# Kernel optimization log

Hardware: AMD Instinct MI355X
Metric: run time of the kernel (lower is better)

The kernel has to match this reference:

```python
import jax, jax.numpy as jnp
import numpy as np

B, L, D_MODEL = 2, 2048, 1024
D_STATE, D_CONV, EXPAND = 8, 4, 2
D_INNER = EXPAND * D_MODEL          # 2048
DT_RANK = (D_MODEL + 15) // 16      # 64


def setup_inputs() -> dict:
    key = jax.random.key(0)
    ks = jax.random.split(key, 8)
    s = 0.02
    x = jax.random.normal(ks[0], (B, L, D_MODEL), dtype=jnp.float32)
    W_in = jax.random.normal(ks[1], (D_MODEL, 2 * D_INNER), dtype=jnp.float32) * s
    dw_kernel = jax.random.normal(ks[2], (D_CONV, D_INNER), dtype=jnp.float32) * s  # depthwise
    pw_kernel = jax.random.normal(ks[3], (D_INNER, D_INNER), dtype=jnp.float32) * s  # pointwise
    conv_bias = jnp.zeros((D_INNER,), dtype=jnp.float32)
    W_x = jax.random.normal(ks[4], (D_INNER, DT_RANK + 2 * D_STATE), dtype=jnp.float32) * s
    W_dt = jax.random.normal(ks[5], (DT_RANK, D_INNER), dtype=jnp.float32) * s
    b_dt = jnp.zeros((D_INNER,), dtype=jnp.float32)
    # A = repeat(range(1..d_state), d_inner).reshape(d_inner, d_state), stored as log
    A_init = np.repeat(np.arange(1, D_STATE + 1, dtype=np.float32), D_INNER).reshape(D_INNER, D_STATE)
    A_log = jnp.asarray(np.log(A_init))
    D = jnp.ones((D_INNER,), dtype=jnp.float32)
    W_out = jax.random.normal(ks[6], (D_INNER, D_MODEL), dtype=jnp.float32) * s
    return {"x": x, "W_in": W_in, "dw_kernel": dw_kernel, "pw_kernel": pw_kernel,
            "conv_bias": conv_bias, "W_x": W_x, "W_dt": W_dt, "b_dt": b_dt,
            "A_log": A_log, "D": D, "W_out": W_out}


def reference(x, W_in, dw_kernel, pw_kernel, conv_bias, W_x, W_dt, b_dt, A_log, D, W_out):
    d_inner, d_state = A_log.shape
    dt_rank = W_dt.shape[0]
    d_conv = dw_kernel.shape[0]
    bsz = x.shape[0]

    xz = x @ W_in                                   # [B,L,2*di]
    x_in, z = jnp.split(xz, 2, axis=-1)             # each [B,L,di]

    # causal separable conv: depthwise (causal pad) -> pointwise -> swish
    xp = jnp.pad(x_in, ((0, 0), (d_conv - 1, 0), (0, 0)))
    xc = jax.lax.conv_general_dilated(
        xp, dw_kernel[:, None, :], window_strides=(1,), padding='VALID',
        dimension_numbers=('NWC', 'WIO', 'NWC'), feature_group_count=d_inner)
    xc = jax.nn.silu(xc @ pw_kernel + conv_bias)    # [B,L,di]

    x_dbl = xc @ W_x                                # [B,L,dt_rank+2*ds]
    delta = x_dbl[..., :dt_rank]
    Bm = x_dbl[..., dt_rank:dt_rank + d_state]      # [B,L,ds]
    C = x_dbl[..., dt_rank + d_state:]              # [B,L,ds]
    delta = jax.nn.softplus(delta @ W_dt + b_dt)    # [B,L,di]

    A = -jnp.exp(A_log)                             # [di,ds]
    deltaA = jnp.exp(jnp.einsum('bld,dn->bldn', delta, A))       # [B,L,di,ds]
    deltaB_u = jnp.einsum('bld,bln,bld->bldn', delta, Bm, xc)    # [B,L,di,ds]

    def step(h, inp):
        dA_t, dBu_t, C_t = inp
        h = dA_t * h + dBu_t                        # [B,di,ds]
        y_t = jnp.einsum('bn,bdn->bd', C_t, h)      # [B,di]
        return h, y_t

    h0 = jnp.zeros((bsz, d_inner, d_state), dtype=x.dtype)
    elems = (deltaA.transpose(1, 0, 2, 3), deltaB_u.transpose(1, 0, 2, 3), C.transpose(1, 0, 2))
    _, ys = jax.lax.scan(step, h0, elems)           # ys: [L,B,di]
    y = ys.transpose(1, 0, 2)                       # [B,L,di]

    y = y + xc * D
    y = y * jax.nn.silu(z)
    return y @ W_out                                # [B,L,d_model]
```

## Files before the change

kernel.cpp:

```cpp
#include <hip/hip_runtime.h>
#include <math.h>

#define Bb 2
#define Ll 2048
#define DMODEL 1024
#define DINNER 2048
#define DSTATE 8
#define DTRANK 64
#define DCONV 4
#define MM (Bb*Ll)
#define NCH 64
#define CL 32
#define G3_KCH 8
#define G3_KC (DINNER / G3_KCH)

typedef __attribute__((ext_vector_type(8))) short    bf16x8;
typedef __attribute__((ext_vector_type(4))) float    f32x4;

__device__ __forceinline__ float silu_f(float x) {
    return x / (1.0f + __expf(-x));
}
__device__ __forceinline__ float softplus_f(float x) {
    return fmaxf(x, 0.0f) + log1pf(__expf(-fabsf(x)));
}
__device__ __forceinline__ unsigned short f2bf(float f) {
    unsigned int u = __float_as_uint(f);
    u += 0x7fffu + ((u >> 16) & 1u);
    return (unsigned short)(u >> 16);
}
__device__ __forceinline__ float bf2f(unsigned short u) {
    return __uint_as_float(((unsigned int)u) << 16);
}
__device__ __forceinline__ void async_cp16(const unsigned short* g, unsigned short* l) {
    __builtin_amdgcn_global_load_lds(
        (const __attribute__((address_space(1))) void*)g,
        (__attribute__((address_space(3))) void*)l, 16, 0, 0);
}

template <int EPI, int NW, int TN, typename OT, int RX = 0, int RY = 1>
__global__ __launch_bounds__(NW * 64, 4) void mfma_gemm(
    const unsigned short* __restrict__ A, const unsigned short* __restrict__ Bt,
    OT* __restrict__ C, OT* __restrict__ C2, int nsplit,
    int M, int N, int K, int lda, int ldb, int ldc,
    const float* __restrict__ bias)
{
    constexpr int NT   = NW * 64;
    constexpr int WNC  = NW / 2;
    constexpr int WNE  = TN / WNC;
    constexpr int NJ   = WNE / 16;
    constexpr int RPP  = NT / 4;
    constexpr int APASS = 128 / RPP;
    constexpr int BPASS = TN / RPP;

    __shared__ unsigned short As[2][128 * 32];
    __shared__ unsigned short Bs[2][TN * 32];

    int bxx = blockIdx.x, byy = blockIdx.y;
    if constexpr (RX > 0) {
        const int f = blockIdx.y * gridDim.x + blockIdx.x;
        const int c = f & 7, q = f >> 3;
        const int rgw = gridDim.x / RX;
        bxx = (c % rgw) * RX + (q % RX);
        byy = (c / rgw) * RY + (q / RX);
    }
    const int bm = byy * 128;
    const int bn = bxx * TN;
    const int tid  = threadIdx.x;
    const int w    = tid >> 6;
    const int lane = tid & 63;
    const int wm = (w / WNC) * 64;
    const int wn = (w % WNC) * WNE;
    const int lr = lane & 15;
    const int lq = lane >> 4;

    const int row  = tid >> 2;
    const int sp   = tid & 3;
    const int slog = sp ^ ((row >> 1) & 3);
    const unsigned short* gA = A  + (size_t)(bm + row) * lda + slog * 8;
    const unsigned short* gB = Bt + (size_t)(bn + row) * ldb + slog * 8;
    const int st = tid * 8;

    const int fsw = (lq ^ ((lr >> 1) & 3)) * 8;

    f32x4 acc[4][NJ];
#pragma unroll
    for (int i = 0; i < 4; ++i)
#pragma unroll
        for (int j = 0; j < NJ; ++j) acc[i][j] = (f32x4){0.f, 0.f, 0.f, 0.f};

#pragma unroll
    for (int p = 0; p < APASS; ++p)
        async_cp16(gA + (size_t)p * RPP * lda, &As[0][p * RPP * 32 + st]);
#pragma unroll
    for (int p = 0; p < BPASS; ++p)
        async_cp16(gB + (size_t)p * RPP * ldb, &Bs[0][p * RPP * 32 + st]);

    int cur = 0;
    for (int k0 = 0; k0 < K; k0 += 32, cur ^= 1) {
        __syncthreads();
        const int nk = k0 + 32;
        if (nk < K) {
            const int nb = cur ^ 1;
#pragma unroll
            for (int p = 0; p < APASS; ++p)
                async_cp16(gA + (size_t)p * RPP * lda + nk, &As[nb][p * RPP * 32 + st]);
#pragma unroll
            for (int p = 0; p < BPASS; ++p)
                async_cp16(gB + (size_t)p * RPP * ldb + nk, &Bs[nb][p * RPP * 32 + st]);
        }

        bf16x8 a[4], b[NJ];
#pragma unroll
        for (int i = 0; i < 4; ++i)
            a[i] = *(const bf16x8*)&As[cur][(wm + i * 16 + lr) * 32 + fsw];
#pragma unroll
        for (int j = 0; j < NJ; ++j)
            b[j] = *(const bf16x8*)&Bs[cur][(wn + j * 16 + lr) * 32 + fsw];
#pragma unroll
        for (int i = 0; i < 4; ++i)
#pragma unroll
            for (int j = 0; j < NJ; ++j)
                acc[i][j] = __builtin_amdgcn_mfma_f32_16x16x32_bf16(
                    a[i], b[j], acc[i][j], 0, 0, 0);
    }

#pragma unroll
    for (int i = 0; i < 4; ++i) {
        const int row0 = bm + wm + i * 16 + lq * 4;
#pragma unroll
        for (int j = 0; j < NJ; ++j) {
            const int col = bn + wn + j * 16 + lr;
            OT* Cb; int colb;
            if (col < nsplit) { Cb = C; colb = col; }
            else              { Cb = C2; colb = col - nsplit; }
            float bv = (EPI != 0) ? bias[col] : 0.0f;
#pragma unroll
            for (int r = 0; r < 4; ++r) {
                float v = acc[i][j][r];
                if (EPI == 1) v = silu_f(v + bv);
                if (EPI == 2) v = softplus_f(v + bv);
                if (sizeof(OT) == 2)
                    Cb[(size_t)(row0 + r) * ldc + colb] = (OT)f2bf(v);
                else
                    Cb[(size_t)(row0 + r) * ldc + colb] = (OT)v;
            }
        }
    }
}

template <bool I1, bool I2, int VMA, int VMB>
__device__ __forceinline__ void g1_tile(
    int kt, const unsigned short* __restrict__ gA,
    const unsigned short* __restrict__ gB, int lda, int ldb,
    unsigned short* As, unsigned short* Bs, int st,
    int wm, int wn, int lr, int fsw, f32x4 (&acc)[8][4])
{
    const int cur = kt & 1;
    const int sb0 = (cur << 1) * 8192;
    const int sb1 = ((cur << 1) | 1) * 8192;
    const int nb1 = ((kt + 1) & 1) << 1;
    const int nb2 = ((kt + 2) & 1) << 1;
    bf16x8 a[4], b[4];

#pragma unroll
    for (int i = 0; i < 4; ++i)
        a[i] = *(const bf16x8*)&As[sb0 + (wm + i * 16 + lr) * 32 + fsw];
#pragma unroll
    for (int j = 0; j < 4; ++j)
        b[j] = *(const bf16x8*)&Bs[sb0 + (wn + j * 16 + lr) * 32 + fsw];
    if (I1) {
        const unsigned short* s = gA + (kt + 1) * 64 + 32;
        unsigned short* d = &As[(nb1 | 1) * 8192 + st];
        async_cp16(s, d);
        async_cp16(s + (size_t)128 * lda, d + 4096);
        __builtin_amdgcn_sched_barrier(0);
    }
    __builtin_amdgcn_s_barrier();
    asm volatile("s_waitcnt lgkmcnt(0)" ::: "memory");
    __builtin_amdgcn_sched_barrier(0);
    __builtin_amdgcn_s_setprio(1);
#pragma unroll
    for (int i = 0; i < 4; ++i)
#pragma unroll
        for (int j = 0; j < 4; ++j)
            acc[i][j] = __builtin_amdgcn_mfma_f32_16x16x32_bf16(
                a[i], b[j], acc[i][j], 0, 0, 0);
    __builtin_amdgcn_s_setprio(0);
    __builtin_amdgcn_s_barrier();

#pragma unroll
    for (int i = 0; i < 4; ++i)
        a[i] = *(const bf16x8*)&As[sb0 + (wm + (4 + i) * 16 + lr) * 32 + fsw];
    if (I1) {
        const unsigned short* s = gB + (kt + 1) * 64 + 32;
        unsigned short* d = &Bs[(nb1 | 1) * 8192 + st];
        async_cp16(s, d);
        async_cp16(s + (size_t)128 * ldb, d + 4096);
        __builtin_amdgcn_sched_barrier(0);
    }
    __builtin_amdgcn_s_barrier();
    asm volatile("s_waitcnt lgkmcnt(0)" ::: "memory");
    __builtin_amdgcn_sched_barrier(0);
    __builtin_amdgcn_s_setprio(1);
#pragma unroll
    for (int i = 0; i < 4; ++i)
#pragma unroll
        for (int j = 0; j < 4; ++j)
            acc[4 + i][j] = __builtin_amdgcn_mfma_f32_16x16x32_bf16(
                a[i], b[j], acc[4 + i][j], 0, 0, 0);
    __builtin_amdgcn_s_setprio(0);
    asm volatile("s_waitcnt vmcnt(%0)" :: "n"(VMA) : "memory");
    __builtin_amdgcn_s_barrier();

#pragma unroll
    for (int i = 0; i < 4; ++i)
        a[i] = *(const bf16x8*)&As[sb1 + (wm + i * 16 + lr) * 32 + fsw];
#pragma unroll
    for (int j = 0; j < 4; ++j)
        b[j] = *(const bf16x8*)&Bs[sb1 + (wn + j * 16 + lr) * 32 + fsw];
    if (I2) {
        const unsigned short* s = gA + (kt + 2) * 64;
        unsigned short* d = &As[nb2 * 8192 + st];
        async_cp16(s, d);
        async_cp16(s + (size_t)128 * lda, d + 4096);
        __builtin_amdgcn_sched_barrier(0);
    }
    __builtin_amdgcn_s_barrier();
    asm volatile("s_waitcnt lgkmcnt(0)" ::: "memory");
    __builtin_amdgcn_sched_barrier(0);
    __builtin_amdgcn_s_setprio(1);
#pragma unroll
    for (int i = 0; i < 4; ++i)
#pragma unroll
        for (int j = 0; j < 4; ++j)
            acc[i][j] = __builtin_amdgcn_mfma_f32_16x16x32_bf16(
                a[i], b[j], acc[i][j], 0, 0, 0);
    __builtin_amdgcn_s_setprio(0);
    __builtin_amdgcn_s_barrier();

#pragma unroll
    for (int i = 0; i < 4; ++i)
        a[i] = *(const bf16x8*)&As[sb1 + (wm + (4 + i) * 16 + lr) * 32 + fsw];
    if (I2) {
        const unsigned short* s = gB + (kt + 2) * 64;
        unsigned short* d = &Bs[nb2 * 8192 + st];
        async_cp16(s, d);
        async_cp16(s + (size_t)128 * ldb, d + 4096);
        __builtin_amdgcn_sched_barrier(0);
    }
    __builtin_amdgcn_s_barrier();
    asm volatile("s_waitcnt lgkmcnt(0)" ::: "memory");
    __builtin_amdgcn_sched_barrier(0);
    __builtin_amdgcn_s_setprio(1);
#pragma unroll
    for (int i = 0; i < 4; ++i)
#pragma unroll
        for (int j = 0; j < 4; ++j)
            acc[4 + i][j] = __builtin_amdgcn_mfma_f32_16x16x32_bf16(
                a[i], b[j], acc[4 + i][j], 0, 0, 0);
    __builtin_amdgcn_s_setprio(0);
    asm volatile("s_waitcnt vmcnt(%0)" :: "n"(VMB) : "memory");
    __builtin_amdgcn_s_barrier();
}

__global__ __launch_bounds__(512, 2) void gemm256_g1(
    const unsigned short* __restrict__ A, const unsigned short* __restrict__ Bt,
    unsigned short* __restrict__ Cx, unsigned short* __restrict__ Cz,
    int K, int lda, int ldb, int ldc, int nsplit)
{
    __shared__ unsigned short As[4 * 8192];
    __shared__ unsigned short Bs[4 * 8192];

    int bx, by;
    {
        const int f = blockIdx.y * gridDim.x + blockIdx.x;
        const int c = f & 7, q = f >> 3;
        const int rgw = gridDim.x >> 3;
        bx = (c % rgw) * 8 + (q & 7);
        by = (c / rgw) * 4 + (q >> 3);
    }
    const int bm = by * 256, bn = bx * 256;
    const int tid  = threadIdx.x;
    const int lane = tid & 63;
    const int w    = tid >> 6;
    const int wm = (w >> 2) << 7;
    const int wn = (w & 3) << 6;
    const int lr = lane & 15;
    const int lq = lane >> 4;
    const int fsw = (lq ^ ((lr >> 1) & 3)) * 8;

    const int row  = tid >> 2;
    const int slog = (tid & 3) ^ ((row >> 1) & 3);
    const unsigned short* gA = A  + (size_t)(bm + row) * lda + slog * 8;
    const unsigned short* gB = Bt + (size_t)(bn + row) * ldb + slog * 8;
    const int st = tid * 8;
    const int NT = K >> 6;

    f32x4 acc[8][4];
#pragma unroll
    for (int i = 0; i < 8; ++i)
#pragma unroll
        for (int j = 0; j < 4; ++j) acc[i][j] = (f32x4){0.f, 0.f, 0.f, 0.f};

    auto stg = [&](const unsigned short* g, int ld, unsigned short* d) {
        async_cp16(g, d);
        async_cp16(g + (size_t)128 * ld, d + 4096);
    };
    stg(gA,      lda, As + 0 * 8192 + st);
    __builtin_amdgcn_sched_barrier(0);
    stg(gB,      ldb, Bs + 0 * 8192 + st);
    __builtin_amdgcn_sched_barrier(0);
    stg(gA + 32, lda, As + 1 * 8192 + st);
    __builtin_amdgcn_sched_barrier(0);
    stg(gB + 32, ldb, Bs + 1 * 8192 + st);
    __builtin_amdgcn_sched_barrier(0);
    stg(gA + 64, lda, As + 2 * 8192 + st);
    __builtin_amdgcn_sched_barrier(0);
    stg(gB + 64, ldb, Bs + 2 * 8192 + st);
    asm volatile("s_waitcnt vmcnt(8)" ::: "memory");
    __builtin_amdgcn_sched_barrier(0);
    __builtin_amdgcn_s_barrier();

    for (int kt = 0; kt + 2 < NT; ++kt)
        g1_tile<true, true, 8, 8>(kt, gA, gB, lda, ldb,
                                  As, Bs, st, wm, wn, lr, fsw, acc);
    g1_tile<true,  false, 8, 4>(NT - 2, gA, gB, lda, ldb,
                                As, Bs, st, wm, wn, lr, fsw, acc);
    g1_tile<false, false, 0, 0>(NT - 1, gA, gB, lda, ldb,
                                As, Bs, st, wm, wn, lr, fsw, acc);

#pragma unroll
    for (int i = 0; i < 8; ++i) {
        const int row0 = bm + wm + i * 16 + lq * 4;
#pragma unroll
        for (int j = 0; j < 4; ++j) {
            const int col = bn + wn + j * 16 + lr;
            unsigned short* Cb; int colb;
            if (col < nsplit) { Cb = Cx; colb = col; }
            else              { Cb = Cz; colb = col - nsplit; }
#pragma unroll
            for (int r = 0; r < 4; ++r)
                Cb[(size_t)(row0 + r) * ldc + colb] = f2bf(acc[i][j][r]);
        }
    }
}

template <bool I1, bool I2, int VMA, int VMB>
__device__ __forceinline__ void g2_tile(
    int kt, const unsigned short* __restrict__ gA,
    const unsigned short* __restrict__ gB, int lda, int ldb,
    unsigned short* As, unsigned short* Bs, int st,
    int wm, int wn, int lr, int fsw, f32x4 (&acc)[4][4])
{
    const int cur = kt & 1;
    const int sa0 = (cur << 1) * 8192;
    const int sa1 = ((cur << 1) | 1) * 8192;
    const int sb0 = (cur << 1) * 4096;
    const int sb1 = ((cur << 1) | 1) * 4096;
    const int nb1 = (((kt + 1) & 1) << 1) | 1;
    const int nb2 = ((kt + 2) & 1) << 1;
    bf16x8 a[4], b[4];

#pragma unroll
    for (int i = 0; i < 4; ++i)
        a[i] = *(const bf16x8*)&As[sa0 + (wm + i * 16 + lr) * 32 + fsw];
#pragma unroll
    for (int j = 0; j < 4; ++j)
        b[j] = *(const bf16x8*)&Bs[sb0 + (wn + j * 16 + lr) * 32 + fsw];
    if (I1) {
        const unsigned short* sA = gA + (kt + 1) * 64 + 32;
        unsigned short* dA = &As[nb1 * 8192 + st];
        async_cp16(sA, dA);
        async_cp16(sA + (size_t)128 * lda, dA + 4096);
        async_cp16(gB + (kt + 1) * 64 + 32, &Bs[nb1 * 4096 + st]);
        __builtin_amdgcn_sched_barrier(0);
    }
    __builtin_amdgcn_s_barrier();
    asm volatile("s_waitcnt lgkmcnt(0)" ::: "memory");
    __builtin_amdgcn_sched_barrier(0);
    __builtin_amdgcn_s_setprio(1);
#pragma unroll
    for (int i = 0; i < 4; ++i)
#pragma unroll
        for (int j = 0; j < 4; ++j)
            acc[i][j] = __builtin_amdgcn_mfma_f32_16x16x32_bf16(
                a[i], b[j], acc[i][j], 0, 0, 0);
    __builtin_amdgcn_s_setprio(0);
    asm volatile("s_waitcnt vmcnt(%0)" :: "n"(VMA) : "memory");
    __builtin_amdgcn_s_barrier();

#pragma unroll
    for (int i = 0; i < 4; ++i)
        a[i] = *(const bf16x8*)&As[sa1 + (wm + i * 16 + lr) * 32 + fsw];
#pragma unroll
    for (int j = 0; j < 4; ++j)
        b[j] = *(const bf16x8*)&Bs[sb1 + (wn + j * 16 + lr) * 32 + fsw];
    if (I2) {
        const unsigned short* sA = gA + (kt + 2) * 64;
        unsigned short* dA = &As[nb2 * 8192 + st];
        async_cp16(sA, dA);
        async_cp16(sA + (size_t)128 * lda, dA + 4096);
        async_cp16(gB + (kt + 2) * 64, &Bs[nb2 * 4096 + st]);
        __builtin_amdgcn_sched_barrier(0);
    }
    __builtin_amdgcn_s_barrier();
    asm volatile("s_waitcnt lgkmcnt(0)" ::: "memory");
    __builtin_amdgcn_sched_barrier(0);
    __builtin_amdgcn_s_setprio(1);
#pragma unroll
    for (int i = 0; i < 4; ++i)
#pragma unroll
        for (int j = 0; j < 4; ++j)
            acc[i][j] = __builtin_amdgcn_mfma_f32_16x16x32_bf16(
                a[i], b[j], acc[i][j], 0, 0, 0);
    __builtin_amdgcn_s_setprio(0);
    asm volatile("s_waitcnt vmcnt(%0)" :: "n"(VMB) : "memory");
    __builtin_amdgcn_s_barrier();
}

template <int EPI, typename OT>
__global__ __launch_bounds__(512, 2) void gemm256x128(
    const unsigned short* __restrict__ A, const unsigned short* __restrict__ Bt,
    OT* __restrict__ C, int K, int lda, int ldb, int ldc,
    const float* __restrict__ bias)
{
    __shared__ unsigned short As[4 * 8192];
    __shared__ unsigned short Bs[4 * 4096];

    int bx, by;
    {
        const int f = blockIdx.y * gridDim.x + blockIdx.x;
        const int c = f & 7, q = f >> 3;
        const int rgw = gridDim.x >> 3;
        bx = (c % rgw) * 8 + (q & 7);
        by = (c / rgw) * 4 + (q >> 3);
    }
    const int bm = by * 256, bn = bx * 128;
    const int tid  = threadIdx.x;
    const int lane = tid & 63;
    const int w    = tid >> 6;
    const int wm = (w >> 1) << 6;
    const int wn = (w & 1) << 6;
    const int lr = lane & 15;
    const int lq = lane >> 4;
    const int fsw = (lq ^ ((lr >> 1) & 3)) * 8;

    const int row  = tid >> 2;
    const int slog = (tid & 3) ^ ((row >> 1) & 3);
    const unsigned short* gA = A  + (size_t)(bm + row) * lda + slog * 8;
    const unsigned short* gB = Bt + (size_t)(bn + row) * ldb + slog * 8;
    const int st = tid * 8;
    const int NT = K >> 6;

    f32x4 acc[4][4];
#pragma unroll
    for (int i = 0; i < 4; ++i)
#pragma unroll
        for (int j = 0; j < 4; ++j) acc[i][j] = (f32x4){0.f, 0.f, 0.f, 0.f};

    auto stg = [&](int ko, int slot) {
        const unsigned short* sA = gA + ko;
        unsigned short* dA = &As[slot * 8192 + st];
        async_cp16(sA, dA);
        async_cp16(sA + (size_t)128 * lda, dA + 4096);
        async_cp16(gB + ko, &Bs[slot * 4096 + st]);
    };
    stg(0, 0);
    __builtin_amdgcn_sched_barrier(0);
    stg(32, 1);
    __builtin_amdgcn_sched_barrier(0);
    stg(64, 2);
    asm volatile("s_waitcnt vmcnt(6)" ::: "memory");
    __builtin_amdgcn_sched_barrier(0);
    __builtin_amdgcn_s_barrier();

    for (int kt = 0; kt + 2 < NT; ++kt)
        g2_tile<true, true, 6, 6>(kt, gA, gB, lda, ldb,
                                  As, Bs, st, wm, wn, lr, fsw, acc);
    g2_tile<true,  false, 6, 3>(NT - 2, gA, gB, lda, ldb,
                                As, Bs, st, wm, wn, lr, fsw, acc);
    g2_tile<false, false, 0, 0>(NT - 1, gA, gB, lda, ldb,
                                As, Bs, st, wm, wn, lr, fsw, acc);

#pragma unroll
    for (int i = 0; i < 4; ++i) {
        const int row0 = bm + wm + i * 16 + lq * 4;
#pragma unroll
        for (int j = 0; j < 4; ++j) {
            const int col = bn + wn + j * 16 + lr;
            float bv = (EPI != 0) ? bias[col] : 0.0f;
#pragma unroll
            for (int r = 0; r < 4; ++r) {
                float v = acc[i][j][r];
                if (EPI == 1) v = silu_f(v + bv);
                if (EPI == 2) v = softplus_f(v + bv);
                if (sizeof(OT) == 2)
                    C[(size_t)(row0 + r) * ldc + col] = (OT)f2bf(v);
                else
                    C[(size_t)(row0 + r) * ldc + col] = (OT)v;
            }
        }
    }
}

__global__ __launch_bounds__(256) void prep_all(
    const float* __restrict__ x, const float* __restrict__ W_in,
    const float* __restrict__ pwk, const float* __restrict__ W_out,
    const float* __restrict__ W_dt,
    unsigned short* __restrict__ x_bf, unsigned short* __restrict__ Wint,
    unsigned short* __restrict__ pw_t, unsigned short* __restrict__ Woutt,
    unsigned short* __restrict__ Wdtt)
{
    const int b = blockIdx.x;
    const int t = threadIdx.x;
    if (b < 4096) {
        int i = b * 1024 + t * 4;
        float4 v = *(const float4*)&x[i];
        ushort4 o;
        o.x = f2bf(v.x); o.y = f2bf(v.y); o.z = f2bf(v.z); o.w = f2bf(v.w);
        *(ushort4*)&x_bf[i] = o;
        return;
    }
    const float* src; unsigned short* dst; int R, C, c0, r0;
    if (b < 8192) {
        int bi = b - 4096; src = W_in; dst = Wint; R = 1024; C = 4096;
        c0 = (bi & 127) * 32; r0 = (bi >> 7) * 32;
    } else if (b < 12288) {
        int bi = b - 8192; src = pwk; dst = pw_t; R = 2048; C = 2048;
        c0 = (bi & 63) * 32; r0 = (bi >> 6) * 32;
    } else if (b < 14336) {
        int bi = b - 12288; src = W_out; dst = Woutt; R = 2048; C = 1024;
        c0 = (bi & 31) * 32; r0 = (bi >> 5) * 32;
    } else {
        int bi = b - 14336; src = W_dt; dst = Wdtt; R = 64; C = 2048;
        c0 = (bi & 63) * 32; r0 = (bi >> 6) * 32;
    }
    __shared__ float tile[32][33];
    const int tx = t & 31;
    const int ty = t >> 5;
#pragma unroll
    for (int i = 0; i < 32; i += 8)
        tile[ty + i][tx] = src[(size_t)(r0 + ty + i) * C + c0 + tx];
    __syncthreads();
#pragma unroll
    for (int i = 0; i < 32; i += 8)
        dst[(size_t)(c0 + ty + i) * R + r0 + tx] = f2bf(tile[tx][ty + i]);
}

__global__ __launch_bounds__(256) void g3_splitk(
    const unsigned short* __restrict__ xc, const float* __restrict__ Wx,
    float* __restrict__ part)
{
    __shared__ float As[16][68];
    __shared__ float Bs[16][85];
    const int m0 = blockIdx.x * 64;
    const int kb = blockIdx.y * G3_KC;
    const int t = threadIdx.x;
    const int tr = t >> 4;
    const int tc = t & 15;

    const int arow = t >> 2;
    const int ak4  = (t & 3) * 4;
    const int bk   = t >> 4;
    const int bc   = (t & 15) * 5;

    float acc[4][5];
#pragma unroll
    for (int r = 0; r < 4; ++r)
#pragma unroll
        for (int c = 0; c < 5; ++c) acc[r][c] = 0.0f;

    for (int k0 = 0; k0 < G3_KC; k0 += 16) {
        ushort4 av = *(const ushort4*)&xc[(size_t)(m0 + arow) * DINNER + kb + k0 + ak4];
        float bv[5];
#pragma unroll
        for (int q = 0; q < 5; ++q)
            bv[q] = Wx[(size_t)(kb + k0 + bk) * 80 + bc + q];
        __syncthreads();
        As[ak4 + 0][arow] = bf2f(av.x);
        As[ak4 + 1][arow] = bf2f(av.y);
        As[ak4 + 2][arow] = bf2f(av.z);
        As[ak4 + 3][arow] = bf2f(av.w);
#pragma unroll
        for (int q = 0; q < 5; ++q) Bs[bk][bc + q] = bv[q];
        __syncthreads();
#pragma unroll
        for (int k = 0; k < 16; ++k) {
            float a[4], b[5];
#pragma unroll
            for (int r = 0; r < 4; ++r) a[r] = As[k][tr * 4 + r];
#pragma unroll
            for (int c = 0; c < 5; ++c) b[c] = Bs[k][tc * 5 + c];
#pragma unroll
            for (int r = 0; r < 4; ++r)
#pragma unroll
                for (int c = 0; c < 5; ++c)
                    acc[r][c] = fmaf(a[r], b[c], acc[r][c]);
        }
    }
#pragma unroll
    for (int r = 0; r < 4; ++r)
#pragma unroll
        for (int c = 0; c < 5; ++c)
            part[((size_t)blockIdx.y * MM + m0 + tr * 4 + r) * 80 + tc * 5 + c] = acc[r][c];
}

__global__ __launch_bounds__(256) void g3_reduce(
    const float* __restrict__ part, float* __restrict__ xdbl,
    unsigned short* __restrict__ xdbl64)
{
    int i = (blockIdx.x * 256 + threadIdx.x) * 4;
    if (i >= MM * 80) return;
    float4 s = *(const float4*)&part[i];
#pragma unroll
    for (int c = 1; c < G3_KCH; ++c) {
        float4 p = *(const float4*)&part[(size_t)c * MM * 80 + i];
        s.x += p.x; s.y += p.y; s.z += p.z; s.w += p.w;
    }
    *(float4*)&xdbl[i] = s;
    int col = i % 80;
    if (col < 64) {
        int row = i / 80;
        ushort4 o;
        o.x = f2bf(s.x); o.y = f2bf(s.y); o.z = f2bf(s.z); o.w = f2bf(s.w);
        *(ushort4*)&xdbl64[(size_t)row * 64 + col] = o;
    }
}

__global__ __launch_bounds__(256) void dwconv_kernel(
    const unsigned short* __restrict__ x_in, const float* __restrict__ dwk,
    unsigned short* __restrict__ out)
{
    int i4 = blockIdx.x * 256 + threadIdx.x;
    if (i4 >= MM * DINNER / 4) return;
    int d = (i4 * 4) & (DINNER - 1);
    int bl = (i4 * 4) >> 11;
    int l = bl & (Ll - 1);
    int b = bl >> 11;
    float a0 = 0.f, a1 = 0.f, a2 = 0.f, a3 = 0.f;
#pragma unroll
    for (int k = 0; k < DCONV; ++k) {
        int t = l + k - (DCONV - 1);
        if (t >= 0) {
            ushort4 xv = *(const ushort4*)&x_in[(size_t)(b * Ll + t) * DINNER + d];
            float4 wv = *(const float4*)&dwk[k * DINNER + d];
            a0 = fmaf(bf2f(xv.x), wv.x, a0);
            a1 = fmaf(bf2f(xv.y), wv.y, a1);
            a2 = fmaf(bf2f(xv.z), wv.z, a2);
            a3 = fmaf(bf2f(xv.w), wv.w, a3);
        }
    }
    ushort4 o;
    o.x = f2bf(a0); o.y = f2bf(a1); o.z = f2bf(a2); o.w = f2bf(a3);
    *(ushort4*)&out[i4 * 4] = o;
}

__global__ __launch_bounds__(256) void scan_pass1(
    const float* __restrict__ delta, const unsigned short* __restrict__ xc,
    const float* __restrict__ xdbl, const float* __restrict__ A_log,
    float* __restrict__ cs_a, float* __restrict__ cs_h)
{
    const int d = blockIdx.x * 256 + threadIdx.x;
    const int c = blockIdx.y;
    const int b = blockIdx.z;
    const int t0 = c * CL;

    __shared__ float sB[CL][8];
    {
        int i = threadIdx.x;
        int t = i >> 3, j = i & 7;
        sB[t][j] = xdbl[((size_t)(b * Ll + t0 + t)) * 80 + DTRANK + j];
    }
    __syncthreads();

    float An[8];
#pragma unroll
    for (int n = 0; n < 8; ++n) An[n] = -__expf(A_log[d * 8 + n]);

    float h[8], ap[8];
#pragma unroll
    for (int n = 0; n < 8; ++n) { h[n] = 0.0f; ap[n] = 1.0f; }

    const float* dptr = delta + ((size_t)(b * Ll + t0)) * DINNER + d;
    const unsigned short* xptr = xc + ((size_t)(b * Ll + t0)) * DINNER + d;

#pragma unroll 4
    for (int t = 0; t < CL; ++t) {
        float dl = dptr[(size_t)t * DINNER];
        float xv = bf2f(xptr[(size_t)t * DINNER]);
        float du = dl * xv;
#pragma unroll
        for (int n = 0; n < 8; ++n) {
            float dA = __expf(dl * An[n]);
            h[n] = fmaf(dA, h[n], du * sB[t][n]);
            ap[n] *= dA;
        }
    }

    size_t base = (((size_t)(b * NCH + c)) * 8) * DINNER + d;
#pragma unroll
    for (int n = 0; n < 8; ++n) {
        cs_a[base + (size_t)n * DINNER] = ap[n];
        cs_h[base + (size_t)n * DINNER] = h[n];
    }
}

__global__ __launch_bounds__(256) void scan_pass2(
    const float* __restrict__ cs_a, const float* cs_h, float* hin)
{
    int idx = blockIdx.x * 256 + threadIdx.x;
    if (idx >= Bb * 8 * DINNER) return;
    int d = idx & (DINNER - 1);
    int n = (idx >> 11) & 7;
    int b = idx >> 14;
    float H = 0.0f;
#pragma unroll 4
    for (int c = 0; c < NCH; ++c) {
        size_t o = (((size_t)(b * NCH + c)) * 8 + n) * DINNER + d;
        float a = cs_a[o];
        float hh = cs_h[o];
        hin[o] = H;
        H = fmaf(a, H, hh);
    }
}

__global__ __launch_bounds__(256) void scan_pass3(
    const float* __restrict__ delta, const unsigned short* __restrict__ xc,
    const float* __restrict__ xdbl, const float* __restrict__ A_log,
    const float* __restrict__ hin, const unsigned short* __restrict__ z,
    const float* __restrict__ Dvec, unsigned short* __restrict__ y_bf)
{
    const int d = blockIdx.x * 256 + threadIdx.x;
    const int c = blockIdx.y;
    const int b = blockIdx.z;
    const int t0 = c * CL;

    __shared__ float sB[CL][8];
    __shared__ float sC[CL][8];
    {
        int i = threadIdx.x;
        int t = i >> 4, j = i & 15;
        float v = xdbl[((size_t)(b * Ll + t0 + t)) * 80 + DTRANK + j];
        if (j < 8) sB[t][j] = v; else sC[t][j - 8] = v;
        t = (i + 256) >> 4; j = (i + 256) & 15;
        v = xdbl[((size_t)(b * Ll + t0 + t)) * 80 + DTRANK + j];
        if (j < 8) sB[t][j] = v; else sC[t][j - 8] = v;
    }
    __syncthreads();

    float An[8];
#pragma unroll
    for (int n = 0; n < 8; ++n) An[n] = -__expf(A_log[d * 8 + n]);

    float h[8];
    size_t hbase = (((size_t)(b * NCH + c)) * 8) * DINNER + d;
#pragma unroll
    for (int n = 0; n < 8; ++n) h[n] = hin[hbase + (size_t)n * DINNER];

    const float Dd = Dvec[d];
    const float* dptr = delta + ((size_t)(b * Ll + t0)) * DINNER + d;
    const unsigned short* xptr = xc + ((size_t)(b * Ll + t0)) * DINNER + d;
    const unsigned short* zptr = z + ((size_t)(b * Ll + t0)) * DINNER + d;
    unsigned short* yptr = y_bf + ((size_t)(b * Ll + t0)) * DINNER + d;

    for (int t = 0; t < CL; ++t) {
        float dl = dptr[(size_t)t * DINNER];
        float xv = bf2f(xptr[(size_t)t * DINNER]);
        float du = dl * xv;
        float yt = 0.0f;
#pragma unroll
        for (int n = 0; n < 8; ++n) {
            float dA = __expf(dl * An[n]);
            h[n] = fmaf(dA, h[n], du * sB[t][n]);
            yt = fmaf(sC[t][n], h[n], yt);
        }
        float zv = bf2f(zptr[(size_t)t * DINNER]);
        yptr[(size_t)t * DINNER] = f2bf((yt + xv * Dd) * silu_f(zv));
    }
}

extern "C" void kernel_launch(void* const* d_in, const int* in_sizes, int n_in,
                              void* d_out, int out_size, void* d_ws, size_t ws_size,
                              hipStream_t stream)
{
    const float* x         = (const float*)d_in[0];
    const float* W_in      = (const float*)d_in[1];
    const float* dwk       = (const float*)d_in[2];
    const float* pwk       = (const float*)d_in[3];
    const float* conv_bias = (const float*)d_in[4];
    const float* W_x       = (const float*)d_in[5];
    const float* W_dt      = (const float*)d_in[6];
    const float* b_dt      = (const float*)d_in[7];
    const float* A_log     = (const float*)d_in[8];
    const float* Dv        = (const float*)d_in[9];
    const float* W_out     = (const float*)d_in[10];
    float* out = (float*)d_out;

    char* ws = (char*)d_ws;
    unsigned short* x_in_bf = (unsigned short*)(ws);
    unsigned short* z_bf    = (unsigned short*)(ws + (16ull << 20));
    float*          delta   = (float*)(ws + (32ull << 20));
    unsigned short* x_bf    = (unsigned short*)(ws + (64ull << 20));
    unsigned short* y_bf    = (unsigned short*)(ws + (64ull << 20));
    unsigned short* Wint    = (unsigned short*)(ws + (72ull << 20));
    unsigned short* pw_t    = (unsigned short*)(ws + (80ull << 20));
    unsigned short* xcp_bf  = (unsigned short*)(ws + (88ull << 20));
    unsigned short* xc_bf   = (unsigned short*)(ws + (104ull << 20));
    unsigned short* Woutt   = (unsigned short*)(ws + (120ull << 20));
    float*          xdbl    = (float*)(ws + (124ull << 20));
    unsigned short* xdbl64  = (unsigned short*)(ws + (125ull << 20) + (512ull << 10));
    float*          g3part  = (float*)(ws + (126ull << 20));
    float*          cs_a    = (float*)(ws + (136ull << 20));
    float*          cs_h    = (float*)(ws + (144ull << 20));
    unsigned short* Wdtt    = (unsigned short*)(ws + (152ull << 20));
    float*          hin     = cs_h;
    dim3 blk(256);

    prep_all<<<14464, blk, 0, stream>>>(x, W_in, pwk, W_out, W_dt,
                                        x_bf, Wint, pw_t, Woutt, Wdtt);

    gemm256_g1<<<dim3((2 * DINNER) / 256, MM / 256), dim3(512), 0, stream>>>(
        x_bf, Wint, x_in_bf, z_bf,
        DMODEL, DMODEL, DMODEL, DINNER,
        DINNER);

    dwconv_kernel<<<MM * DINNER / 4 / 256, blk, 0, stream>>>(x_in_bf, dwk, xcp_bf);

    gemm256x128<1, unsigned short>
        <<<dim3(DINNER / 128, MM / 256), dim3(512), 0, stream>>>(
        xcp_bf, pw_t, xc_bf,
        DINNER, DINNER, DINNER, DINNER, conv_bias);

    g3_splitk<<<dim3(MM / 64, G3_KCH), blk, 0, stream>>>(xc_bf, W_x, g3part);
    g3_reduce<<<(MM * 80 / 4 + 255) / 256, blk, 0, stream>>>(g3part, xdbl, xdbl64);

    mfma_gemm<2, 4, 128, float, 8, 8>
        <<<dim3(DINNER / 128, MM / 128), blk, 0, stream>>>(
        xdbl64, Wdtt, delta, delta, DINNER + 1,
        MM, DINNER, DTRANK, DTRANK, DTRANK, DINNER, b_dt);

    scan_pass1<<<dim3(DINNER / 256, NCH, Bb), blk, 0, stream>>>(
        delta, xc_bf, xdbl, A_log, cs_a, cs_h);
    scan_pass2<<<(Bb * 8 * DINNER + 255) / 256, blk, 0, stream>>>(cs_a, cs_h, hin);
    scan_pass3<<<dim3(DINNER / 256, NCH, Bb), blk, 0, stream>>>(
        delta, xc_bf, xdbl, A_log, hin, z_bf, Dv, y_bf);

    mfma_gemm<0, 4, 64, float, 8, 8>
        <<<dim3(DMODEL / 64, MM / 128), blk, 0, stream>>>(
        y_bf, Woutt, out, out, DMODEL + 1,
        MM, DMODEL, DINNER, DINNER, DINNER, DMODEL, nullptr);
}
```

Baseline: 362.8 us.

## Triple-buffer LDS in gemm256x128 to cut barriers to one per k-tile

```diff
diff --git a/kernel.cpp b/kernel.cpp
--- a/kernel.cpp
+++ b/kernel.cpp
@@ -345,37 +345,35 @@
     }
 }
 
-template <bool I1, bool I2, int VMA, int VMB>
-__device__ __forceinline__ void g2_tile(
+template <bool STG, int VM>
+__device__ __forceinline__ void g2b_tile(
     int kt, const unsigned short* __restrict__ gA,
     const unsigned short* __restrict__ gB, int lda, int ldb,
     unsigned short* As, unsigned short* Bs, int st,
     int wm, int wn, int lr, int fsw, f32x4 (&acc)[4][4])
 {
-    const int cur = kt & 1;
-    const int sa0 = (cur << 1) * 8192;
-    const int sa1 = ((cur << 1) | 1) * 8192;
-    const int sb0 = (cur << 1) * 4096;
-    const int sb1 = ((cur << 1) | 1) * 4096;
-    const int nb1 = (((kt + 1) & 1) << 1) | 1;
-    const int nb2 = ((kt + 2) & 1) << 1;
+    const int buf  = kt % 3;
+    const int buf2 = (kt + 2) % 3;
+    unsigned short* A0 = As + (buf * 2 + 0) * 8192;
+    unsigned short* A1 = As + (buf * 2 + 1) * 8192;
+    unsigned short* B0 = Bs + (buf * 2 + 0) * 4096;
+    unsigned short* B1 = Bs + (buf * 2 + 1) * 4096;
     bf16x8 a[4], b[4];
 
 #pragma unroll
     for (int i = 0; i < 4; ++i)
-        a[i] = *(const bf16x8*)&As[sa0 + (wm + i * 16 + lr) * 32 + fsw];
+        a[i] = *(const bf16x8*)&A0[(wm + i * 16 + lr) * 32 + fsw];
 #pragma unroll
     for (int j = 0; j < 4; ++j)
-        b[j] = *(const bf16x8*)&Bs[sb0 + (wn + j * 16 + lr) * 32 + fsw];
-    if (I1) {
-        const unsigned short* sA = gA + (kt + 1) * 64 + 32;
-        unsigned short* dA = &As[nb1 * 8192 + st];
+        b[j] = *(const bf16x8*)&B0[(wn + j * 16 + lr) * 32 + fsw];
+    if (STG) {
+        const unsigned short* sA = gA + (kt + 2) * 64;
+        unsigned short* dA = As + (buf2 * 2 + 0) * 8192 + st;
         async_cp16(sA, dA);
         async_cp16(sA + (size_t)128 * lda, dA + 4096);
-        async_cp16(gB + (kt + 1) * 64 + 32, &Bs[nb1 * 4096 + st]);
+        async_cp16(gB + (kt + 2) * 64, Bs + (buf2 * 2 + 0) * 4096 + st);
         __builtin_amdgcn_sched_barrier(0);
     }
-    __builtin_amdgcn_s_barrier();
     asm volatile("s_waitcnt lgkmcnt(0)" ::: "memory");
     __builtin_amdgcn_sched_barrier(0);
     __builtin_amdgcn_s_setprio(1);
@@ -386,24 +384,21 @@
             acc[i][j] = __builtin_amdgcn_mfma_f32_16x16x32_bf16(
                 a[i], b[j], acc[i][j], 0, 0, 0);
     __builtin_amdgcn_s_setprio(0);
-    asm volatile("s_waitcnt vmcnt(%0)" :: "n"(VMA) : "memory");
-    __builtin_amdgcn_s_barrier();
-
-#pragma unroll
-    for (int i = 0; i < 4; ++i)
-        a[i] = *(const bf16x8*)&As[sa1 + (wm + i * 16 + lr) * 32 + fsw];
+
+#pragma unroll
+    for (int i = 0; i < 4; ++i)
+        a[i] = *(const bf16x8*)&A1[(wm + i * 16 + lr) * 32 + fsw];
 #pragma unroll
     for (int j = 0; j < 4; ++j)
-        b[j] = *(const bf16x8*)&Bs[sb1 + (wn + j * 16 + lr) * 32 + fsw];
-    if (I2) {
-        const unsigned short* sA = gA + (kt + 2) * 64;
-        unsigned short* dA = &As[nb2 * 8192 + st];
+        b[j] = *(const bf16x8*)&B1[(wn + j * 16 + lr) * 32 + fsw];
+    if (STG) {
+        const unsigned short* sA = gA + (kt + 2) * 64 + 32;
+        unsigned short* dA = As + (buf2 * 2 + 1) * 8192 + st;
         async_cp16(sA, dA);
         async_cp16(sA + (size_t)128 * lda, dA + 4096);
-        async_cp16(gB + (kt + 2) * 64, &Bs[nb2 * 4096 + st]);
+        async_cp16(gB + (kt + 2) * 64 + 32, Bs + (buf2 * 2 + 1) * 4096 + st);
         __builtin_amdgcn_sched_barrier(0);
     }
-    __builtin_amdgcn_s_barrier();
     asm volatile("s_waitcnt lgkmcnt(0)" ::: "memory");
     __builtin_amdgcn_sched_barrier(0);
     __builtin_amdgcn_s_setprio(1);
@@ -414,8 +409,11 @@
             acc[i][j] = __builtin_amdgcn_mfma_f32_16x16x32_bf16(
                 a[i], b[j], acc[i][j], 0, 0, 0);
     __builtin_amdgcn_s_setprio(0);
-    asm volatile("s_waitcnt vmcnt(%0)" :: "n"(VMB) : "memory");
-    __builtin_amdgcn_s_barrier();
+
+    if constexpr (VM >= 0) {
+        asm volatile("s_waitcnt vmcnt(%0)" :: "n"(VM) : "memory");
+        __builtin_amdgcn_s_barrier();
+    }
 }
 
 template <int EPI, typename OT>
@@ -424,8 +422,8 @@
     OT* __restrict__ C, int K, int lda, int ldb, int ldc,
     const float* __restrict__ bias)
 {
-    __shared__ unsigned short As[4 * 8192];
-    __shared__ unsigned short Bs[4 * 4096];
+    __shared__ unsigned short As[6 * 8192];
+    __shared__ unsigned short Bs[6 * 4096];
 
     int bx, by;
     {
@@ -460,27 +458,29 @@
 
     auto stg = [&](int ko, int slot) {
         const unsigned short* sA = gA + ko;
-        unsigned short* dA = &As[slot * 8192 + st];
+        unsigned short* dA = As + slot * 8192 + st;
         async_cp16(sA, dA);
         async_cp16(sA + (size_t)128 * lda, dA + 4096);
-        async_cp16(gB + ko, &Bs[slot * 4096 + st]);
+        async_cp16(gB + ko, Bs + slot * 4096 + st);
     };
     stg(0, 0);
     __builtin_amdgcn_sched_barrier(0);
     stg(32, 1);
     __builtin_amdgcn_sched_barrier(0);
     stg(64, 2);
+    __builtin_amdgcn_sched_barrier(0);
+    stg(96, 3);
     asm volatile("s_waitcnt vmcnt(6)" ::: "memory");
     __builtin_amdgcn_sched_barrier(0);
     __builtin_amdgcn_s_barrier();
 
-    for (int kt = 0; kt + 2 < NT; ++kt)
-        g2_tile<true, true, 6, 6>(kt, gA, gB, lda, ldb,
-                                  As, Bs, st, wm, wn, lr, fsw, acc);
-    g2_tile<true,  false, 6, 3>(NT - 2, gA, gB, lda, ldb,
-                                As, Bs, st, wm, wn, lr, fsw, acc);
-    g2_tile<false, false, 0, 0>(NT - 1, gA, gB, lda, ldb,
-                                As, Bs, st, wm, wn, lr, fsw, acc);
+    for (int kt = 0; kt < NT - 2; ++kt)
+        g2b_tile<true, 6>(kt, gA, gB, lda, ldb,
+                          As, Bs, st, wm, wn, lr, fsw, acc);
+    g2b_tile<false, 0>(NT - 2, gA, gB, lda, ldb,
+                       As, Bs, st, wm, wn, lr, fsw, acc);
+    g2b_tile<false, -1>(NT - 1, gA, gB, lda, ldb,
+                        As, Bs, st, wm, wn, lr, fsw, acc);
 
 #pragma unroll
     for (int i = 0; i < 4; ++i) {
```

Measured after the change: 410.2 us. 13.1% more time.
